# Optimization experiments

Measured on AMD Instinct MI355X. Metric: run time of the kernel, lower is better.

The kernel has to match this reference:

```python
import jax, jax.numpy as jnp
import numpy as np

H = 256  # hidden_dim
B, T, F = 128, 512, 256  # batch, seq_len, input features (= hidden_dim)
LN_EPS = 1e-3  # keras LayerNormalization default epsilon


def _lstm_layer(x, W, U, b):
    """Keras LSTM, return_sequences=True, inference (no dropout).
    x: [B,T,D], W: [D,4H], U: [H,4H], b: [4H]. Gate order: i,f,g(c),o."""
    xz = jnp.einsum('btd,dk->btk', x, W) + b  # [B,T,4H] input projections
    xz_t = jnp.swapaxes(xz, 0, 1)  # [T,B,4H]
    h0 = jnp.zeros((x.shape[0], U.shape[0]), x.dtype)
    c0 = jnp.zeros_like(h0)

    def step(carry, z_in):
        h, c = carry
        z = z_in + h @ U  # [B,4H]
        i, f, g, o = jnp.split(z, 4, axis=-1)
        i = jax.nn.sigmoid(i)
        f = jax.nn.sigmoid(f)
        g = jnp.tanh(g)
        o = jax.nn.sigmoid(o)
        c = f * c + i * g
        h = o * jnp.tanh(c)
        return (h, c), h

    _, hs = jax.lax.scan(step, (h0, c0), xz_t)  # hs: [T,B,H]
    return jnp.swapaxes(hs, 0, 1)  # [B,T,H]


def setup_inputs() -> dict:
    key = jax.random.key(0)
    ks = jax.random.split(key, 12)
    s_in = 1.0 / np.sqrt(F)
    s_h = 1.0 / np.sqrt(H)
    inp = {
        'x': jax.random.normal(ks[0], (B, T, F), jnp.float32),
        'W0': jax.random.normal(ks[1], (F, 4 * H), jnp.float32) * s_in,
        'U0': jax.random.normal(ks[2], (H, 4 * H), jnp.float32) * s_h,
        'b0': jnp.zeros((4 * H,), jnp.float32),
        'W1': jax.random.normal(ks[3], (H, 4 * H), jnp.float32) * s_h,
        'U1': jax.random.normal(ks[4], (H, 4 * H), jnp.float32) * s_h,
        'b1': jnp.zeros((4 * H,), jnp.float32),
        'Wd': jax.random.normal(ks[5], (H, H), jnp.float32) * s_h,
        'bd': jnp.zeros((H,), jnp.float32),
        'gamma': jnp.ones((H,), jnp.float32),
        'beta': jnp.zeros((H,), jnp.float32),
    }
    return inp


def reference(x, W0, U0, b0, W1, U1, b1, Wd, bd, gamma, beta):
    h = _lstm_layer(x, W0, U0, b0)
    h = _lstm_layer(h, W1, U1, b1)
    h = jnp.tanh(jnp.einsum('bth,hk->btk', h, Wd) + bd)  # Dense(tanh)
    mu = jnp.mean(h, axis=-1, keepdims=True)
    var = jnp.mean(jnp.square(h - mu), axis=-1, keepdims=True)
    return (h - mu) * jax.lax.rsqrt(var + LN_EPS) * gamma + beta
```

## Files before the change

### kernel.cpp

```cpp
#include <hip/hip_runtime.h>
#include <stdint.h>

#define B_ 128
#define T_ 512
#define H_ 256
#define CH 32
#define NC 16
#define RB 32
#define CSRC ((size_t)CH * 32768)

typedef short bf16x8 __attribute__((ext_vector_type(8)));
typedef float f32x4 __attribute__((ext_vector_type(4)));
typedef int   i32x4 __attribute__((ext_vector_type(4)));

__device__ __forceinline__ unsigned short f2bf(float f) {
    union { float f; uint32_t u; } v; v.f = f;
    uint32_t u = v.u;
    return (unsigned short)((u + 0x7FFFu + ((u >> 16) & 1u)) >> 16);
}
__device__ __forceinline__ float bf2f(unsigned int b) {
    union { uint32_t u; float f; } v; v.u = (b & 0xFFFFu) << 16; return v.f;
}
__device__ __forceinline__ float sigm(float x) { return 1.0f / (1.0f + __expf(-x)); }
__device__ __forceinline__ float tanh_(float x) { return 1.0f - 2.0f / (__expf(2.0f * x) + 1.0f); }

__global__ void k_prep_x(const float* __restrict__ x, unsigned short* __restrict__ xbf) {
    int idx = blockIdx.x * blockDim.x + threadIdx.x;
    int f4 = idx & 63;
    int t = (idx >> 6) & 511;
    int b = idx >> 15;
    float4 v = *(const float4*)(x + ((size_t)b * T_ + t) * H_ + f4 * 4);
    ushort4 o;
    o.x = f2bf(v.x); o.y = f2bf(v.y); o.z = f2bf(v.z); o.w = f2bf(v.w);
    *(ushort4*)(xbf + ((size_t)t * B_ + b) * H_ + f4 * 4) = o;
}

__global__ void k_prep_w(const float* __restrict__ in, unsigned short* __restrict__ out) {
    int idx = blockIdx.x * blockDim.x + threadIdx.x;
    int k = idx & 255; int col = idx >> 8;
    out[(size_t)col * 256 + k] = f2bf(in[(size_t)k * 1024 + col]);
}

__global__ void k_prep_wd(const float* __restrict__ Wd, unsigned short* __restrict__ Wdt) {
    int idx = blockIdx.x * blockDim.x + threadIdx.x;
    int k = idx & 255; int col = idx >> 8;
    Wdt[(size_t)col * 256 + k] = f2bf(Wd[(size_t)k * 256 + col]);
}

__global__ void k_umax(const float* __restrict__ in, float* __restrict__ slot) {
    float m = 0.f;
    for (int i = blockIdx.x * blockDim.x + threadIdx.x; i < 262144; i += gridDim.x * blockDim.x)
        m = fmaxf(m, fabsf(in[i]));
#pragma unroll
    for (int off = 1; off < 64; off <<= 1) m = fmaxf(m, __shfl_xor(m, off));
    if ((threadIdx.x & 63) == 0) atomicMax((int*)slot, __float_as_int(m));
}

__global__ void k_prep_u(const float* __restrict__ in, const float* __restrict__ umax,
                         signed char* __restrict__ out) {
    int idx = blockIdx.x * blockDim.x + threadIdx.x;
    int k = idx & 255; int col = idx >> 8;
    float s = 127.f / *umax;
    float v = in[(size_t)k * 1024 + col] * s;
    out[(size_t)col * 256 + k] = (signed char)__float2int_rn(fminf(fmaxf(v, -127.f), 127.f));
}


__device__ __forceinline__ void gemm_path(
    int ob, int tid,
    const unsigned short* __restrict__ A, const unsigned short* __restrict__ Bt,
    const float* __restrict__ bias, unsigned short* __restrict__ xz) {
    const int tl = ob >> 2, nq = ob & 3;
    const int wave = tid >> 6, lane = tid & 63, quad = lane >> 4, l15 = lane & 15;
    const f32x4 zero = {0.f, 0.f, 0.f, 0.f};
    f32x4 acc[2][16];
#pragma unroll
    for (int m = 0; m < 2; ++m)
#pragma unroll
        for (int n = 0; n < 16; ++n) acc[m][n] = zero;

#pragma unroll
    for (int kt = 0; kt < 8; ++kt) {
        bf16x8 a0 = *(const bf16x8*)(A + ((size_t)(tl * 128 + wave * 32 + l15)) * 256 + kt * 32 + quad * 8);
        bf16x8 a1 = *(const bf16x8*)(A + ((size_t)(tl * 128 + wave * 32 + 16 + l15)) * 256 + kt * 32 + quad * 8);
#pragma unroll
        for (int ntl = 0; ntl < 16; ++ntl) {
            bf16x8 b = *(const bf16x8*)(Bt + ((size_t)(nq * 256 + ntl * 16 + l15)) * 256 + kt * 32 + quad * 8);
            acc[0][ntl] = __builtin_amdgcn_mfma_f32_16x16x32_bf16(a0, b, acc[0][ntl], 0, 0, 0);
            acc[1][ntl] = __builtin_amdgcn_mfma_f32_16x16x32_bf16(a1, b, acc[1][ntl], 0, 0, 0);
        }
    }
#pragma unroll
    for (int ntl = 0; ntl < 16; ++ntl) {
        int c0 = nq * 256 + ntl * 16;
        float bv = bias[c0 + l15];
        int wr = ntl >> 2, s = ntl & 3;
        int n = nq * 4 + s;
#pragma unroll
        for (int mt = 0; mt < 2; ++mt) {
            int rg = wave * 2 + mt;
            unsigned long long pk = 0;
#pragma unroll
            for (int r = 0; r < 4; ++r)
                pk |= ((unsigned long long)f2bf(acc[mt][ntl][r] + bv)) << (16 * r);
            *(unsigned long long*)(xz + (((size_t)(tl * 8 + rg) * 4 + wr) * 16 + n) * 256 + lane * 4) = pk;
        }
    }
}

__device__ __forceinline__ void rec_path(
    int blk, int tid,
    const signed char* __restrict__ Ui8,
    const unsigned short* __restrict__ xz,
    const float* __restrict__ uscale,
    unsigned short* __restrict__ hout,
    float* __restrict__ cstate,
    int t0) {
    __shared__ __align__(16) int zbuf[4096];
    __shared__ __align__(16) signed char hbuf[2][16 * 272];
    const int w = tid >> 6, lane = tid & 63, quad = lane >> 4, l15 = lane & 15;
    const int sh = quad * 16;
    const int wr = w >> 1;
    const int whalf = w & 1;
    const int colbase = wr * 64 + whalf * 32;

    i32x4 Bf[8][4];
#pragma unroll
    for (int n = 0; n < 8; ++n) {
        int col = (n >> 1) * 256 + colbase + (n & 1) * 16 + l15;
#pragma unroll
        for (int kt = 0; kt < 4; ++kt)
            Bf[n][kt] = *(const i32x4*)(Ui8 + (size_t)col * 256 + kt * 64 + quad * 16);
    }

    for (int i = tid; i < 2176; i += 512) ((int*)hbuf)[i] = 0;

    float cst[2];
    if (t0 > 0) {
#pragma unroll
        for (int s = 0; s < 2; ++s) {
            int col = colbase + s * 16 + l15;
            float h = bf2f(hout[((size_t)(t0 - 1) * 128 + blk * 4 + quad) * 256 + col]);
            hbuf[0][quad * 272 + col] = (signed char)__float2int_rn(h * 127.f);
            cst[s] = cstate[(size_t)blk * 1024 + tid * 2 + s];
        }
    } else {
        cst[0] = 0.f; cst[1] = 0.f;
    }
    const float SUH = (*uscale) * (1.f / 16129.f);
    __syncthreads();

    const i32x4 zeroi = {0, 0, 0, 0};
    int p = 0;
#pragma unroll 1
    for (int tl = 0; tl < CH; ++tl) {
        const unsigned short* xb = xz + (size_t)tl * 131072 + (blk >> 2) * 16384
                                      + wr * 4096 + (blk & 3) * 64 + l15 * 4;
        unsigned long long xu[8];
#pragma unroll
        for (int n = 0; n < 8; ++n) {
            int n_old = (n >> 1) * 4 + whalf * 2 + (n & 1);
            xu[n] = *(const unsigned long long*)(xb + n_old * 256);
        }

        const signed char* hb = hbuf[p];
        i32x4 Af[4];
#pragma unroll
        for (int kt = 0; kt < 4; ++kt)
            Af[kt] = *(const i32x4*)(hb + l15 * 272 + kt * 64 + quad * 16);

        i32x4 acc[8];
#pragma unroll
        for (int n = 0; n < 8; ++n) acc[n] = zeroi;
#pragma unroll
        for (int kt = 0; kt < 4; ++kt) {
            i32x4 a = Af[kt];
#pragma unroll
            for (int n = 0; n < 8; ++n)
                acc[n] = __builtin_amdgcn_mfma_i32_16x16x64_i8(a, Bf[n][kt], acc[n], 0, 0, 0);
        }

        if (quad == 0) {
#pragma unroll
            for (int n = 0; n < 8; ++n)
                *(i32x4*)(zbuf + ((w * 8 + n) * 16 + l15) * 4) = acc[n];
        }
        float zv[8];
#pragma unroll
        for (int n = 0; n < 8; ++n) {
            int zi = zbuf[((w * 8 + n) * 16 + l15) * 4 + quad];
            zv[n] = (float)zi * SUH + bf2f((unsigned int)(xu[n] >> sh));
        }

        unsigned short* hO = hout + ((size_t)((t0 + tl) * 128 + blk * 4 + quad)) * 256 + colbase + l15;
        signed char* hw = hbuf[p ^ 1];
#pragma unroll
        for (int s = 0; s < 2; ++s) {
            float c = sigm(zv[2 + s]) * cst[s] + sigm(zv[s]) * tanh_(zv[4 + s]);
            cst[s] = c;
            float h = sigm(zv[6 + s]) * tanh_(c);
            hw[quad * 272 + colbase + s * 16 + l15] = (signed char)__float2int_rn(h * 127.f);
            hO[s * 16] = f2bf(h);
        }
        asm volatile("s_waitcnt lgkmcnt(0)" ::: "memory");
        __builtin_amdgcn_s_barrier();
        asm volatile("" ::: "memory");
        p ^= 1;
    }
#pragma unroll
    for (int s = 0; s < 2; ++s)
        cstate[(size_t)blk * 1024 + tid * 2 + s] = cst[s];
}

__device__ __forceinline__ void dense_path(
    int t, int tid,
    const unsigned short* __restrict__ h2buf, const unsigned short* __restrict__ Wdt,
    const float* __restrict__ bd, const float* __restrict__ gamma,
    const float* __restrict__ beta, float* __restrict__ out) {
    const int wave = tid >> 6, lane = tid & 63, quad = lane >> 4, l15 = lane & 15;
    const unsigned short* A = h2buf + (size_t)t * B_ * H_;
    const f32x4 zero = {0.f, 0.f, 0.f, 0.f};

    f32x4 acc[2][16];
#pragma unroll
    for (int m = 0; m < 2; ++m)
#pragma unroll
        for (int n = 0; n < 16; ++n) acc[m][n] = zero;

#pragma unroll
    for (int kt = 0; kt < 8; ++kt) {
        bf16x8 a[2];
#pragma unroll
        for (int m = 0; m < 2; ++m) {
            int row = wave * 32 + m * 16 + l15;
            a[m] = *(const bf16x8*)(A + (size_t)row * H_ + kt * 32 + quad * 8);
        }
#pragma unroll
        for (int n = 0; n < 16; ++n) {
            bf16x8 b = *(const bf16x8*)(Wdt + (size_t)(n * 16 + l15) * H_ + kt * 32 + quad * 8);
            acc[0][n] = __builtin_amdgcn_mfma_f32_16x16x32_bf16(a[0], b, acc[0][n], 0, 0, 0);
            acc[1][n] = __builtin_amdgcn_mfma_f32_16x16x32_bf16(a[1], b, acc[1][n], 0, 0, 0);
        }
    }

    float gm[16], bt[16], bdv[16];
#pragma unroll
    for (int n = 0; n < 16; ++n) {
        int c = n * 16 + l15;
        gm[n] = gamma[c]; bt[n] = beta[c]; bdv[n] = bd[c];
    }
#pragma unroll
    for (int m = 0; m < 2; ++m) {
#pragma unroll
        for (int r = 0; r < 4; ++r) {
            float v[16], s = 0.f, sq = 0.f;
#pragma unroll
            for (int n = 0; n < 16; ++n) {
                float x = tanh_(acc[m][n][r] + bdv[n]);
                v[n] = x; s += x; sq += x * x;
            }
#pragma unroll
            for (int off = 1; off < 16; off <<= 1) {
                s += __shfl_xor(s, off);
                sq += __shfl_xor(sq, off);
            }
            float mu = s * (1.f / 256.f);
            float var = sq * (1.f / 256.f) - mu * mu;
            float rs = rsqrtf(var + 1e-3f);
            int row = wave * 32 + m * 16 + quad * 4 + r;
            float* po = out + (size_t)row * (T_ * H_) + (size_t)t * H_;
#pragma unroll
            for (int n = 0; n < 16; ++n)
                po[n * 16 + l15] = (v[n] - mu) * rs * gm[n] + bt[n];
        }
    }
}

__global__ __launch_bounds__(512, 2) void k_fused(
    const signed char* __restrict__ U0i8, const unsigned short* __restrict__ xz0,
    const float* __restrict__ us0, unsigned short* __restrict__ ho0,
    float* __restrict__ cs0, int t00, int nr0,
    const signed char* __restrict__ U1i8, const unsigned short* __restrict__ xz1,
    const float* __restrict__ us1, unsigned short* __restrict__ ho1,
    float* __restrict__ cs1, int t01, int nr1,
    const unsigned short* __restrict__ g0A, const unsigned short* __restrict__ g0B,
    const float* __restrict__ g0b, unsigned short* __restrict__ g0x, int ng0,
    const unsigned short* __restrict__ g1A, const unsigned short* __restrict__ g1B,
    const float* __restrict__ g1b, unsigned short* __restrict__ g1x, int ng1,
    const unsigned short* __restrict__ dH, const unsigned short* __restrict__ dWdt,
    const float* __restrict__ dbd, const float* __restrict__ dgamma,
    const float* __restrict__ dbeta, float* __restrict__ dout, int tbase, int nd) {
    int bid = blockIdx.x;
    const int tid = threadIdx.x;
    if (bid < nr0) {
        rec_path(bid, tid, U0i8, xz0, us0, ho0, cs0, t00);
        return;
    }
    bid -= nr0;
    if (bid < nr1) {
        rec_path(bid, tid, U1i8, xz1, us1, ho1, cs1, t01);
        return;
    }
    bid -= nr1;
    if (bid < ng0) {
        gemm_path(bid * 2 + (tid >> 8), tid & 255, g0A, g0B, g0b, g0x);
        return;
    }
    bid -= ng0;
    if (bid < ng1) {
        gemm_path(bid * 2 + (tid >> 8), tid & 255, g1A, g1B, g1b, g1x);
        return;
    }
    bid -= ng1;
    if (bid < nd) {
        dense_path(tbase + bid * 2 + (tid >> 8), tid & 255, dH, dWdt, dbd, dgamma, dbeta, dout);
    }
}

extern "C" void kernel_launch(void* const* d_in, const int* in_sizes, int n_in,
                              void* d_out, int out_size, void* d_ws, size_t ws_size,
                              hipStream_t stream) {
    const float* x     = (const float*)d_in[0];
    const float* W0    = (const float*)d_in[1];
    const float* U0    = (const float*)d_in[2];
    const float* b0    = (const float*)d_in[3];
    const float* W1    = (const float*)d_in[4];
    const float* U1    = (const float*)d_in[5];
    const float* b1    = (const float*)d_in[6];
    const float* Wd    = (const float*)d_in[7];
    const float* bd    = (const float*)d_in[8];
    const float* gamma = (const float*)d_in[9];
    const float* beta  = (const float*)d_in[10];
    float* out = (float*)d_out;

    char* ws = (char*)d_ws;
    const bool big = ws_size >= (99ull << 20);

    unsigned short* buf0 = (unsigned short*)(ws);
    unsigned short* h1   = (unsigned short*)(ws + (32u << 20));
    unsigned short* xz0s[2], *xz1s[2];
    size_t tail;
    if (big) {
        xz0s[0] = (unsigned short*)(ws + (64u << 20));
        xz0s[1] = (unsigned short*)(ws + (72u << 20));
        xz1s[0] = (unsigned short*)(ws + (80u << 20));
        xz1s[1] = (unsigned short*)(ws + (88u << 20));
        tail = (size_t)96 << 20;
    } else {
        xz0s[0] = (unsigned short*)(ws + (64u << 20));
        xz0s[1] = xz0s[0];
        xz1s[0] = (unsigned short*)(ws + (72u << 20));
        xz1s[1] = xz1s[0];
        tail = (size_t)80 << 20;
    }
    unsigned short* Wt0  = (unsigned short*)(ws + tail);
    unsigned short* Wt1  = (unsigned short*)(ws + tail + 524288);
    signed char*    Ui0  = (signed char*)  (ws + tail + 1048576);
    signed char*    Ui1  = (signed char*)  (ws + tail + 1310720);
    unsigned short* Wdt  = (unsigned short*)(ws + tail + 1572864);
    float*          sc   = (float*)        (ws + tail + 1703936);
    float*          cb0  = (float*)        (ws + tail + 1704448);
    float*          cb1  = (float*)        (ws + tail + 1835520);

    hipMemsetAsync(sc, 0, 64, stream);
    k_prep_x<<<16384, 256, 0, stream>>>(x, buf0);
    k_prep_w<<<1024, 256, 0, stream>>>(W0, Wt0);
    k_prep_w<<<1024, 256, 0, stream>>>(W1, Wt1);
    k_prep_wd<<<256, 256, 0, stream>>>(Wd, Wdt);
    k_umax<<<256, 256, 0, stream>>>(U0, sc);
    k_umax<<<256, 256, 0, stream>>>(U1, sc + 1);
    k_prep_u<<<1024, 256, 0, stream>>>(U0, sc, Ui0);
    k_prep_u<<<1024, 256, 0, stream>>>(U1, sc + 1, Ui1);

    for (int k = 0; k < NC + 4; ++k) {
        int g0 = k, r0 = k - 1, g1 = k - 2, r1 = k - 3, d = k - 4;
        int ng0 = (g0 >= 0 && g0 < NC) ? CH * 2 : 0;
        int nr0 = (r0 >= 0 && r0 < NC) ? RB : 0;
        int ng1 = (g1 >= 0 && g1 < NC) ? CH * 2 : 0;
        int nr1 = (r1 >= 0 && r1 < NC) ? RB : 0;
        int nd  = (d  >= 0 && d  < NC) ? CH / 2 : 0;
        int grid = nr0 + nr1 + ng0 + ng1 + nd;
        if (grid == 0) continue;
        int g0c = g0 < 0 ? 0 : (g0 >= NC ? NC - 1 : g0);
        int r0c = r0 < 0 ? 0 : (r0 >= NC ? NC - 1 : r0);
        int g1c = g1 < 0 ? 0 : (g1 >= NC ? NC - 1 : g1);
        int r1c = r1 < 0 ? 0 : (r1 >= NC ? NC - 1 : r1);
        int dc  = d  < 0 ? 0 : (d  >= NC ? NC - 1 : d);
        k_fused<<<grid, 512, 0, stream>>>(
            Ui0, xz0s[r0c & 1], sc,     h1,   cb0, r0c * CH, nr0,
            Ui1, xz1s[r1c & 1], sc + 1, buf0, cb1, r1c * CH, nr1,
            buf0 + (size_t)g0c * CSRC, Wt0, b0, xz0s[g0c & 1], ng0,
            h1   + (size_t)g1c * CSRC, Wt1, b1, xz1s[g1c & 1], ng1,
            buf0, Wdt, bd, gamma, beta, out, dc * CH, nd);
    }
}
```

Before: 1.274 ms.

## Double block size to 1024 threads, halving per-thread work in all paths

The fused kernel now launches 1024-thread blocks instead of 512. In the recurrent path each wave owns 16 hidden columns with 4 gate tiles instead of 32 columns with 8. The GEMM and dense paths each process one 16-row M tile per wave instead of two. The aim is to shorten the serial per-timestep critical path in the recurrence by spreading each step over more waves, and to cut register pressure. The cost is a larger block barrier across 16 waves, more redundant B-operand loads in the GEMM and dense paths, and one block per CU under the new launch bounds.

```diff
diff --git a/kernel.cpp b/kernel.cpp
--- a/kernel.cpp
+++ b/kernel.cpp
@@ -67,44 +67,35 @@
 
 
 __device__ __forceinline__ void gemm_path(
-    int ob, int tid,
+    int ob, int stid,
     const unsigned short* __restrict__ A, const unsigned short* __restrict__ Bt,
     const float* __restrict__ bias, unsigned short* __restrict__ xz) {
     const int tl = ob >> 2, nq = ob & 3;
-    const int wave = tid >> 6, lane = tid & 63, quad = lane >> 4, l15 = lane & 15;
+    const int w8 = stid >> 6, lane = stid & 63, quad = lane >> 4, l15 = lane & 15;
     const f32x4 zero = {0.f, 0.f, 0.f, 0.f};
-    f32x4 acc[2][16];
-#pragma unroll
-    for (int m = 0; m < 2; ++m)
-#pragma unroll
-        for (int n = 0; n < 16; ++n) acc[m][n] = zero;
+    f32x4 acc[16];
+#pragma unroll
+    for (int n = 0; n < 16; ++n) acc[n] = zero;
 
 #pragma unroll
     for (int kt = 0; kt < 8; ++kt) {
-        bf16x8 a0 = *(const bf16x8*)(A + ((size_t)(tl * 128 + wave * 32 + l15)) * 256 + kt * 32 + quad * 8);
-        bf16x8 a1 = *(const bf16x8*)(A + ((size_t)(tl * 128 + wave * 32 + 16 + l15)) * 256 + kt * 32 + quad * 8);
+        bf16x8 a = *(const bf16x8*)(A + ((size_t)(tl * 128 + w8 * 16 + l15)) * 256 + kt * 32 + quad * 8);
 #pragma unroll
         for (int ntl = 0; ntl < 16; ++ntl) {
             bf16x8 b = *(const bf16x8*)(Bt + ((size_t)(nq * 256 + ntl * 16 + l15)) * 256 + kt * 32 + quad * 8);
-            acc[0][ntl] = __builtin_amdgcn_mfma_f32_16x16x32_bf16(a0, b, acc[0][ntl], 0, 0, 0);
-            acc[1][ntl] = __builtin_amdgcn_mfma_f32_16x16x32_bf16(a1, b, acc[1][ntl], 0, 0, 0);
+            acc[ntl] = __builtin_amdgcn_mfma_f32_16x16x32_bf16(a, b, acc[ntl], 0, 0, 0);
         }
     }
 #pragma unroll
     for (int ntl = 0; ntl < 16; ++ntl) {
-        int c0 = nq * 256 + ntl * 16;
-        float bv = bias[c0 + l15];
+        float bv = bias[nq * 256 + ntl * 16 + l15];
         int wr = ntl >> 2, s = ntl & 3;
         int n = nq * 4 + s;
-#pragma unroll
-        for (int mt = 0; mt < 2; ++mt) {
-            int rg = wave * 2 + mt;
-            unsigned long long pk = 0;
-#pragma unroll
-            for (int r = 0; r < 4; ++r)
-                pk |= ((unsigned long long)f2bf(acc[mt][ntl][r] + bv)) << (16 * r);
-            *(unsigned long long*)(xz + (((size_t)(tl * 8 + rg) * 4 + wr) * 16 + n) * 256 + lane * 4) = pk;
-        }
+        unsigned long long pk = 0;
+#pragma unroll
+        for (int r = 0; r < 4; ++r)
+            pk |= ((unsigned long long)f2bf(acc[ntl][r] + bv)) << (16 * r);
+        *(unsigned long long*)(xz + (((size_t)(tl * 8 + w8) * 4 + wr) * 16 + n) * 256 + lane * 4) = pk;
     }
 }
 
@@ -120,32 +111,26 @@
     __shared__ __align__(16) signed char hbuf[2][16 * 272];
     const int w = tid >> 6, lane = tid & 63, quad = lane >> 4, l15 = lane & 15;
     const int sh = quad * 16;
-    const int wr = w >> 1;
-    const int whalf = w & 1;
-    const int colbase = wr * 64 + whalf * 32;
-
-    i32x4 Bf[8][4];
-#pragma unroll
-    for (int n = 0; n < 8; ++n) {
-        int col = (n >> 1) * 256 + colbase + (n & 1) * 16 + l15;
+    const int col = w * 16 + l15;
+
+    i32x4 Bf[4][4];
+#pragma unroll
+    for (int g = 0; g < 4; ++g) {
+        int zc = g * 256 + col;
 #pragma unroll
         for (int kt = 0; kt < 4; ++kt)
-            Bf[n][kt] = *(const i32x4*)(Ui8 + (size_t)col * 256 + kt * 64 + quad * 16);
-    }
-
-    for (int i = tid; i < 2176; i += 512) ((int*)hbuf)[i] = 0;
-
-    float cst[2];
+            Bf[g][kt] = *(const i32x4*)(Ui8 + (size_t)zc * 256 + kt * 64 + quad * 16);
+    }
+
+    for (int i = tid; i < 2176; i += 1024) ((int*)hbuf)[i] = 0;
+
+    float cst;
     if (t0 > 0) {
-#pragma unroll
-        for (int s = 0; s < 2; ++s) {
-            int col = colbase + s * 16 + l15;
-            float h = bf2f(hout[((size_t)(t0 - 1) * 128 + blk * 4 + quad) * 256 + col]);
-            hbuf[0][quad * 272 + col] = (signed char)__float2int_rn(h * 127.f);
-            cst[s] = cstate[(size_t)blk * 1024 + tid * 2 + s];
-        }
+        float h = bf2f(hout[((size_t)(t0 - 1) * 128 + blk * 4 + quad) * 256 + col]);
+        hbuf[0][quad * 272 + col] = (signed char)__float2int_rn(h * 127.f);
+        cst = cstate[(size_t)blk * 1024 + tid];
     } else {
-        cst[0] = 0.f; cst[1] = 0.f;
+        cst = 0.f;
     }
     const float SUH = (*uscale) * (1.f / 16129.f);
     __syncthreads();
@@ -155,13 +140,11 @@
 #pragma unroll 1
     for (int tl = 0; tl < CH; ++tl) {
         const unsigned short* xb = xz + (size_t)tl * 131072 + (blk >> 2) * 16384
-                                      + wr * 4096 + (blk & 3) * 64 + l15 * 4;
-        unsigned long long xu[8];
-#pragma unroll
-        for (int n = 0; n < 8; ++n) {
-            int n_old = (n >> 1) * 4 + whalf * 2 + (n & 1);
-            xu[n] = *(const unsigned long long*)(xb + n_old * 256);
-        }
+                                      + (w >> 2) * 4096 + (blk & 3) * 64 + l15 * 4;
+        unsigned long long xu[4];
+#pragma unroll
+        for (int g = 0; g < 4; ++g)
+            xu[g] = *(const unsigned long long*)(xb + (g * 4 + (w & 3)) * 256);
 
         const signed char* hb = hbuf[p];
         i32x4 Af[4];
@@ -169,114 +152,90 @@
         for (int kt = 0; kt < 4; ++kt)
             Af[kt] = *(const i32x4*)(hb + l15 * 272 + kt * 64 + quad * 16);
 
-        i32x4 acc[8];
-#pragma unroll
-        for (int n = 0; n < 8; ++n) acc[n] = zeroi;
+        i32x4 acc[4];
+#pragma unroll
+        for (int g = 0; g < 4; ++g) acc[g] = zeroi;
 #pragma unroll
         for (int kt = 0; kt < 4; ++kt) {
             i32x4 a = Af[kt];
 #pragma unroll
-            for (int n = 0; n < 8; ++n)
-                acc[n] = __builtin_amdgcn_mfma_i32_16x16x64_i8(a, Bf[n][kt], acc[n], 0, 0, 0);
+            for (int g = 0; g < 4; ++g)
+                acc[g] = __builtin_amdgcn_mfma_i32_16x16x64_i8(a, Bf[g][kt], acc[g], 0, 0, 0);
         }
 
         if (quad == 0) {
 #pragma unroll
-            for (int n = 0; n < 8; ++n)
-                *(i32x4*)(zbuf + ((w * 8 + n) * 16 + l15) * 4) = acc[n];
-        }
-        float zv[8];
-#pragma unroll
-        for (int n = 0; n < 8; ++n) {
-            int zi = zbuf[((w * 8 + n) * 16 + l15) * 4 + quad];
-            zv[n] = (float)zi * SUH + bf2f((unsigned int)(xu[n] >> sh));
-        }
-
-        unsigned short* hO = hout + ((size_t)((t0 + tl) * 128 + blk * 4 + quad)) * 256 + colbase + l15;
-        signed char* hw = hbuf[p ^ 1];
-#pragma unroll
-        for (int s = 0; s < 2; ++s) {
-            float c = sigm(zv[2 + s]) * cst[s] + sigm(zv[s]) * tanh_(zv[4 + s]);
-            cst[s] = c;
-            float h = sigm(zv[6 + s]) * tanh_(c);
-            hw[quad * 272 + colbase + s * 16 + l15] = (signed char)__float2int_rn(h * 127.f);
-            hO[s * 16] = f2bf(h);
-        }
+            for (int g = 0; g < 4; ++g)
+                *(i32x4*)(zbuf + ((w * 4 + g) * 16 + l15) * 4) = acc[g];
+        }
+        float zv[4];
+#pragma unroll
+        for (int g = 0; g < 4; ++g) {
+            int zi = zbuf[((w * 4 + g) * 16 + l15) * 4 + quad];
+            zv[g] = (float)zi * SUH + bf2f((unsigned int)(xu[g] >> sh));
+        }
+
+        float c = sigm(zv[1]) * cst + sigm(zv[0]) * tanh_(zv[2]);
+        cst = c;
+        float h = sigm(zv[3]) * tanh_(c);
+        hbuf[p ^ 1][quad * 272 + col] = (signed char)__float2int_rn(h * 127.f);
+        hout[((size_t)((t0 + tl) * 128 + blk * 4 + quad)) * 256 + col] = f2bf(h);
+
         asm volatile("s_waitcnt lgkmcnt(0)" ::: "memory");
         __builtin_amdgcn_s_barrier();
         asm volatile("" ::: "memory");
         p ^= 1;
     }
-#pragma unroll
-    for (int s = 0; s < 2; ++s)
-        cstate[(size_t)blk * 1024 + tid * 2 + s] = cst[s];
+    cstate[(size_t)blk * 1024 + tid] = cst;
 }
 
 __device__ __forceinline__ void dense_path(
-    int t, int tid,
+    int t, int stid,
     const unsigned short* __restrict__ h2buf, const unsigned short* __restrict__ Wdt,
     const float* __restrict__ bd, const float* __restrict__ gamma,
     const float* __restrict__ beta, float* __restrict__ out) {
-    const int wave = tid >> 6, lane = tid & 63, quad = lane >> 4, l15 = lane & 15;
+    const int w8 = stid >> 6, lane = stid & 63, quad = lane >> 4, l15 = lane & 15;
     const unsigned short* A = h2buf + (size_t)t * B_ * H_;
     const f32x4 zero = {0.f, 0.f, 0.f, 0.f};
-
-    f32x4 acc[2][16];
-#pragma unroll
-    for (int m = 0; m < 2; ++m)
-#pragma unroll
-        for (int n = 0; n < 16; ++n) acc[m][n] = zero;
-
+    f32x4 acc[16];
+#pragma unroll
+    for (int n = 0; n < 16; ++n) acc[n] = zero;
 #pragma unroll
     for (int kt = 0; kt < 8; ++kt) {
-        bf16x8 a[2];
-#pragma unroll
-        for (int m = 0; m < 2; ++m) {
-            int row = wave * 32 + m * 16 + l15;
-            a[m] = *(const bf16x8*)(A + (size_t)row * H_ + kt * 32 + quad * 8);
-        }
+        bf16x8 a = *(const bf16x8*)(A + (size_t)(w8 * 16 + l15) * H_ + kt * 32 + quad * 8);
 #pragma unroll
         for (int n = 0; n < 16; ++n) {
             bf16x8 b = *(const bf16x8*)(Wdt + (size_t)(n * 16 + l15) * H_ + kt * 32 + quad * 8);
-            acc[0][n] = __builtin_amdgcn_mfma_f32_16x16x32_bf16(a[0], b, acc[0][n], 0, 0, 0);
-            acc[1][n] = __builtin_amdgcn_mfma_f32_16x16x32_bf16(a[1], b, acc[1][n], 0, 0, 0);
-        }
-    }
-
-    float gm[16], bt[16], bdv[16];
-#pragma unroll
-    for (int n = 0; n < 16; ++n) {
-        int c = n * 16 + l15;
-        gm[n] = gamma[c]; bt[n] = beta[c]; bdv[n] = bd[c];
-    }
-#pragma unroll
-    for (int m = 0; m < 2; ++m) {
-#pragma unroll
-        for (int r = 0; r < 4; ++r) {
-            float v[16], s = 0.f, sq = 0.f;
-#pragma unroll
-            for (int n = 0; n < 16; ++n) {
-                float x = tanh_(acc[m][n][r] + bdv[n]);
-                v[n] = x; s += x; sq += x * x;
-            }
-#pragma unroll
-            for (int off = 1; off < 16; off <<= 1) {
-                s += __shfl_xor(s, off);
-                sq += __shfl_xor(sq, off);
-            }
-            float mu = s * (1.f / 256.f);
-            float var = sq * (1.f / 256.f) - mu * mu;
-            float rs = rsqrtf(var + 1e-3f);
-            int row = wave * 32 + m * 16 + quad * 4 + r;
-            float* po = out + (size_t)row * (T_ * H_) + (size_t)t * H_;
-#pragma unroll
-            for (int n = 0; n < 16; ++n)
-                po[n * 16 + l15] = (v[n] - mu) * rs * gm[n] + bt[n];
-        }
-    }
-}
-
-__global__ __launch_bounds__(512, 2) void k_fused(
+            acc[n] = __builtin_amdgcn_mfma_f32_16x16x32_bf16(a, b, acc[n], 0, 0, 0);
+        }
+    }
+#pragma unroll
+    for (int r = 0; r < 4; ++r) {
+        float v[16], s = 0.f, sq = 0.f;
+#pragma unroll
+        for (int n = 0; n < 16; ++n) {
+            float x = tanh_(acc[n][r] + bd[n * 16 + l15]);
+            v[n] = x; s += x; sq += x * x;
+        }
+#pragma unroll
+        for (int off = 1; off < 16; off <<= 1) {
+            s += __shfl_xor(s, off);
+            sq += __shfl_xor(sq, off);
+        }
+        float mu = s * (1.f / 256.f);
+        float var = sq * (1.f / 256.f) - mu * mu;
+        float rs = rsqrtf(var + 1e-3f);
+        int row = w8 * 16 + quad * 4 + r;
+        float* po = out + (size_t)row * (T_ * H_) + (size_t)t * H_;
+#pragma unroll
+        for (int n = 0; n < 16; ++n) {
+            int cc = n * 16 + l15;
+            po[cc] = (v[n] - mu) * rs * gamma[cc] + beta[cc];
+        }
+    }
+}
+
+__global__ __launch_bounds__(1024, 1) void k_fused(
     const signed char* __restrict__ U0i8, const unsigned short* __restrict__ xz0,
     const float* __restrict__ us0, unsigned short* __restrict__ ho0,
     float* __restrict__ cs0, int t00, int nr0,
@@ -303,17 +262,17 @@
     }
     bid -= nr1;
     if (bid < ng0) {
-        gemm_path(bid * 2 + (tid >> 8), tid & 255, g0A, g0B, g0b, g0x);
+        gemm_path(bid * 2 + (tid >> 9), tid & 511, g0A, g0B, g0b, g0x);
         return;
     }
     bid -= ng0;
     if (bid < ng1) {
-        gemm_path(bid * 2 + (tid >> 8), tid & 255, g1A, g1B, g1b, g1x);
+        gemm_path(bid * 2 + (tid >> 9), tid & 511, g1A, g1B, g1b, g1x);
         return;
     }
     bid -= ng1;
     if (bid < nd) {
-        dense_path(tbase + bid * 2 + (tid >> 8), tid & 255, dH, dWdt, dbd, dgamma, dbeta, dout);
+        dense_path(tbase + bid * 2 + (tid >> 9), tid & 511, dH, dWdt, dbd, dgamma, dbeta, dout);
     }
 }
 
@@ -386,7 +345,7 @@
         int g1c = g1 < 0 ? 0 : (g1 >= NC ? NC - 1 : g1);
         int r1c = r1 < 0 ? 0 : (r1 >= NC ? NC - 1 : r1);
         int dc  = d  < 0 ? 0 : (d  >= NC ? NC - 1 : d);
-        k_fused<<<grid, 512, 0, stream>>>(
+        k_fused<<<grid, 1024, 0, stream>>>(
             Ui0, xz0s[r0c & 1], sc,     h1,   cb0, r0c * CH, nr0,
             Ui1, xz1s[r1c & 1], sc + 1, buf0, cb1, r1c * CH, nr1,
             buf0 + (size_t)g0c * CSRC, Wt0, b0, xz0s[g0c & 1], ng0,
```

After: 1.711 ms. 34.3% more time.
